# Performance work log

Hardware: AMD Instinct MI355X
Metric: run time of the kernel (lower is better)

## Reference

```python
import jax, jax.numpy as jnp
import numpy as np

NTOKEN = 32000
NINP = 400
NHID = 1150
SEQ = 70
BATCH = 16
ODE_STEPS = 2  # fixed-step RK4 stand-in for adaptive odeint on t in [0,1]


def setup_inputs() -> dict:
    key = jax.random.key(0)
    ks = jax.random.split(key, 16)
    f32 = jnp.float32

    def rn(k, shape, s=0.05):
        return (jax.random.normal(k, shape) * s).astype(f32)

    inp = {"tokens": jax.random.randint(ks[0], (SEQ, BATCH), 0, NTOKEN)}
    dims = [(NINP, NHID), (NHID, NHID), (NHID, NINP)]  # (in, hidden) per layer
    for l, (din, dh) in enumerate(dims):
        inp[f"h0_{l}"] = jnp.zeros((BATCH, dh), f32)
        inp[f"c0_{l}"] = jnp.zeros((BATCH, dh), f32)
        inp[f"Wih{l}"] = rn(ks[1 + 2 * l], (4 * dh, din))
        inp[f"Whh{l}"] = rn(ks[2 + 2 * l], (4 * dh, dh))
        inp[f"bih{l}"] = jnp.zeros((4 * dh,), f32)
        inp[f"bhh{l}"] = jnp.zeros((4 * dh,), f32)
    inp["emb"] = jax.random.uniform(ks[8], (NTOKEN, NINP), minval=-0.1, maxval=0.1, dtype=f32)
    inp["decW"] = jax.random.uniform(ks[9], (NTOKEN, NINP), minval=-0.1, maxval=0.1, dtype=f32)
    inp["decb"] = jnp.zeros((NTOKEN,), f32)
    # ODEfunc: ConcatLinear over [t, x] (width NTOKEN+1) -> NINP bottleneck -> NTOKEN
    inp["odeW1"] = rn(ks[10], (NINP, NTOKEN + 1), 0.01)
    inp["odeb1"] = jnp.zeros((NINP,), f32)
    inp["odeW2"] = rn(ks[11], (NTOKEN, NINP), 0.01)
    inp["odeb2"] = jnp.zeros((NTOKEN,), f32)
    return inp


def _lstm_layer(x, h0, c0, Wih, Whh, bih, bhh):
    # x: [S, B, din] -> outputs [S, B, H]; PyTorch gate order i, f, g, o.
    xp = jnp.einsum('sbd,gd->sbg', x, Wih) + bih + bhh  # [S, B, 4H]

    def cell(carry, xpt):
        h, c = carry
        g = xpt + h @ Whh.T
        i, f, gg, o = jnp.split(g, 4, axis=-1)
        c = jax.nn.sigmoid(f) * c + jax.nn.sigmoid(i) * jnp.tanh(gg)
        h = jax.nn.sigmoid(o) * jnp.tanh(c)
        return (h, c), h

    (hT, cT), ys = jax.lax.scan(cell, (h0, c0), xp)
    return ys, hT, cT


def _ode_rk4(x, W1, b1, W2, b2, n_steps):
    # ConcatLinear: column 0 of W1 multiplies t, remaining columns multiply x.
    wt = W1[:, 0]   # [bneck]
    Wx = W1[:, 1:]  # [bneck, NTOKEN]

    def f(t, y):
        h = jax.nn.softplus(y @ Wx.T + t * wt + b1)
        return h @ W2.T + b2

    dt = 1.0 / n_steps
    ts = jnp.arange(n_steps, dtype=x.dtype) * dt

    def step(y, t):
        k1 = f(t, y)
        k2 = f(t + 0.5 * dt, y + 0.5 * dt * k1)
        k3 = f(t + 0.5 * dt, y + 0.5 * dt * k2)
        k4 = f(t + dt, y + dt * k3)
        return y + (dt / 6.0) * (k1 + 2.0 * k2 + 2.0 * k3 + k4), None

    y, _ = jax.lax.scan(step, x, ts)
    return y


def _forward(tokens, h0s, c0s, lstm_params, emb, decW, decb, odeW1, odeb1, odeW2, odeb2):
    x = emb[tokens]  # [S, B, NINP]  (eval mode: all dropouts inactive)
    for l, (Wih, Whh, bih, bhh) in enumerate(lstm_params):
        x, _, _ = _lstm_layer(x, h0s[l], c0s[l], Wih, Whh, bih, bhh)
    logit = x @ decW.T + decb              # [S, B, NTOKEN]; nhidlast==ninp so no latent layer
    flat = logit.reshape(-1, NTOKEN)       # ODEfunc operates on 2D [S*B, NTOKEN]
    trans = _ode_rk4(flat, odeW1, odeb1, odeW2, odeb2, ODE_STEPS)
    prob = jax.nn.softmax(trans, axis=-1)
    log_prob = jnp.log(prob + 1e-8)        # matches torch.log(prob + 1e-8)
    return log_prob.reshape(SEQ, BATCH, NTOKEN)


def reference(tokens, h0_0, c0_0, h0_1, c0_1, h0_2, c0_2,
              Wih0, Whh0, bih0, bhh0, Wih1, Whh1, bih1, bhh1,
              Wih2, Whh2, bih2, bhh2,
              emb, decW, decb, odeW1, odeb1, odeW2, odeb2):
    return _forward(tokens,
                    [h0_0, h0_1, h0_2], [c0_0, c0_1, c0_2],
                    [(Wih0, Whh0, bih0, bhh0),
                     (Wih1, Whh1, bih1, bhh1),
                     (Wih2, Whh2, bih2, bhh2)],
                    emb, decW, decb, odeW1, odeb1, odeW2, odeb2)
```

## Files before the change

kernel.cpp:

```cpp
#include <hip/hip_runtime.h>
#include <math.h>

constexpr int S_   = 70;
constexpr int B_   = 16;
constexpr int SB_  = 1120;
constexpr int NT_  = 32000;
constexpr int W1S_ = 32001;
constexpr int AST  = 424;

typedef __attribute__((ext_vector_type(8))) short bf16x8;
typedef __attribute__((ext_vector_type(4))) float f32x4;

__device__ __forceinline__ float sigm(float x){ return 1.f/(1.f+__expf(-x)); }
__device__ __forceinline__ float softplusf(float x){ return x > 15.f ? x : log1pf(__expf(x)); }

__device__ __forceinline__ unsigned short f2bf(float f){
    union{float f; unsigned u;} c; c.f = f;
    unsigned u = c.u;
    unsigned r = (u + 0x7fffu + ((u >> 16) & 1u)) >> 16;
    return (unsigned short)r;
}
__device__ __forceinline__ float bfu(unsigned short us){
    union{unsigned u; float f;} c; c.u = ((unsigned)us) << 16; return c.f;
}

__global__ __launch_bounds__(256) void cvt_pack_all_k(
    const float* __restrict__ s0, unsigned short* __restrict__ d0,
    const float* __restrict__ s1, unsigned short* __restrict__ d1,
    const float* __restrict__ s2, unsigned short* __restrict__ d2,
    const float* __restrict__ s3, unsigned short* __restrict__ d3,
    const float* __restrict__ s4, unsigned short* __restrict__ d4,
    const float* __restrict__ s5, unsigned short* __restrict__ d5)
{
    int seg = blockIdx.y;
    const float* src; unsigned short* dst; int R, K, Kp;
    switch(seg){
      case 0: src=s0; dst=d0; R=4600; K=400;  Kp=416;  break;
      case 1: src=s1; dst=d1; R=4600; K=1150; Kp=1152; break;
      case 2: src=s2; dst=d2; R=4600; K=1150; Kp=1152; break;
      case 3: src=s3; dst=d3; R=4600; K=1150; Kp=1152; break;
      case 4: src=s4; dst=d4; R=1600; K=1150; Kp=1152; break;
      default:src=s5; dst=d5; R=1600; K=400;  Kp=416;  break;
    }
    long long idx = (long long)blockIdx.x*256 + threadIdx.x;
    long long tot = (long long)R*Kp;
    if (idx >= tot) return;
    int r = (int)(idx / Kp), kk = (int)(idx - (long long)r*Kp);
    float v = (kk < K) ? src[(size_t)r*K + kk] : 0.f;
    dst[idx] = f2bf(v);
}

__global__ __launch_bounds__(256) void cvt_catB2_k(const float* __restrict__ decW,
                                                   const float* __restrict__ odeW2,
                                                   unsigned short* __restrict__ Bbf,
                                                   unsigned short* __restrict__ BbfT)
{
    __shared__ unsigned short tile[32][72];
    int v0 = blockIdx.x*64, n0 = blockIdx.y*32;
    int tx = threadIdx.x & 31;
    int vy = threadIdx.x >> 5;
    #pragma unroll
    for (int i = 0; i < 8; ++i){
        int v = v0 + i*8 + vy;
        int n = n0 + tx;
        float val = (n < 400) ? decW[(size_t)v*400 + n] : odeW2[(size_t)v*400 + (n-400)];
        unsigned short us = f2bf(val);
        tile[tx][v - v0] = us;
        Bbf[(size_t)v*800 + n] = us;
    }
    __syncthreads();
    int vx = threadIdx.x & 63;
    int ny = threadIdx.x >> 6;
    #pragma unroll
    for (int i = 0; i < 8; ++i){
        int n = n0 + i*4 + ny;
        BbfT[(size_t)n*NT_ + v0 + vx] = tile[n - n0][vx];
    }
}

__global__ __launch_bounds__(256) void cvt_wx_k(const float* __restrict__ odeW1,
                                                unsigned short* __restrict__ Wxbf)
{
    long long idx = (long long)blockIdx.x*256 + threadIdx.x;
    if (idx >= (long long)400*NT_) return;
    int m = (int)(idx / NT_), v = (int)(idx - (long long)m*NT_);
    Wxbf[idx] = f2bf(odeW1[(size_t)m*W1S_ + 1 + v]);
}

__global__ __launch_bounds__(256) void embed_bf_k(const int* __restrict__ tok,
                                                  const float* __restrict__ emb,
                                                  unsigned short* __restrict__ x0A)
{
    int t = blockIdx.x;
    __shared__ int tk[16];
    if (threadIdx.x < 16) tk[threadIdx.x] = tok[t*16 + threadIdx.x];
    __syncthreads();
    for (int idx = threadIdx.x; idx < 16*416; idx += 256){
        int b = idx / 416, k = idx - b*416;
        float v = (k < 400) ? emb[(size_t)tk[b]*400 + k] : 0.f;
        x0A[(size_t)t*16*416 + idx] = f2bf(v);
    }
}

__global__ __launch_bounds__(256) void transpose16_k(const float* __restrict__ src,
                                                     float* __restrict__ dst, int dh)
{
    int idx = blockIdx.x*256 + threadIdx.x;
    if (idx < dh*16){ int j = idx >> 4, b = idx & 15; dst[idx] = src[b*dh + j]; }
}

__global__ __launch_bounds__(256) void cvt_h0_k(const float* __restrict__ h0,
                                                unsigned short* __restrict__ hb, int Dh, int SA)
{
    int idx = blockIdx.x*256 + threadIdx.x;
    if (idx >= 16*Dh) return;
    int b = idx / Dh, j = idx - b*Dh;
    hb[(size_t)b*SA + j] = f2bf(h0[idx]);
}

__device__ __forceinline__ void dotseg(const unsigned short* __restrict__ a,
                                       const unsigned short* __restrict__ b,
                                       int s, int e, int kq,
                                       f32x4& c0, f32x4& c1, f32x4& c2, f32x4& c3)
{
    int k0 = s;
    for (; k0 + 128 <= e; k0 += 128){
        bf16x8 a0 = *(const bf16x8*)(a + k0 + kq);
        bf16x8 b0 = *(const bf16x8*)(b + k0 + kq);
        bf16x8 a1 = *(const bf16x8*)(a + k0 + 32 + kq);
        bf16x8 b1 = *(const bf16x8*)(b + k0 + 32 + kq);
        bf16x8 a2 = *(const bf16x8*)(a + k0 + 64 + kq);
        bf16x8 b2 = *(const bf16x8*)(b + k0 + 64 + kq);
        bf16x8 a3 = *(const bf16x8*)(a + k0 + 96 + kq);
        bf16x8 b3 = *(const bf16x8*)(b + k0 + 96 + kq);
        c0 = __builtin_amdgcn_mfma_f32_16x16x32_bf16(a0, b0, c0, 0,0,0);
        c1 = __builtin_amdgcn_mfma_f32_16x16x32_bf16(a1, b1, c1, 0,0,0);
        c2 = __builtin_amdgcn_mfma_f32_16x16x32_bf16(a2, b2, c2, 0,0,0);
        c3 = __builtin_amdgcn_mfma_f32_16x16x32_bf16(a3, b3, c3, 0,0,0);
    }
    int rem = e - k0;
    if (rem >= 32){
        bf16x8 a0 = *(const bf16x8*)(a + k0 + kq);
        bf16x8 b0 = *(const bf16x8*)(b + k0 + kq);
        c0 = __builtin_amdgcn_mfma_f32_16x16x32_bf16(a0, b0, c0, 0,0,0);
    }
    if (rem >= 64){
        bf16x8 a1 = *(const bf16x8*)(a + k0 + 32 + kq);
        bf16x8 b1 = *(const bf16x8*)(b + k0 + 32 + kq);
        c1 = __builtin_amdgcn_mfma_f32_16x16x32_bf16(a1, b1, c1, 0,0,0);
    }
    if (rem >= 96){
        bf16x8 a2 = *(const bf16x8*)(a + k0 + 64 + kq);
        bf16x8 b2 = *(const bf16x8*)(b + k0 + 64 + kq);
        c2 = __builtin_amdgcn_mfma_f32_16x16x32_bf16(a2, b2, c2, 0,0,0);
    }
}

__global__ __launch_bounds__(1024) void xproj0_k(const unsigned short* __restrict__ x0A,
                                                 const unsigned short* __restrict__ Wih0p,
                                                 unsigned short* __restrict__ xp0)
{
    int jt = blockIdx.x, t = blockIdx.y;
    int j0 = jt*16;
    int lane = threadIdx.x & 63, w = threadIdx.x >> 6;
    int gate = w & 3, seg = w >> 2;
    int am = lane & 15, kq = (lane >> 4)*8, jn = lane & 15;
    int jrow = j0 + jn; if (jrow > 1149) jrow = 1149;

    const unsigned short* ax = x0A + (size_t)t*16*416 + (size_t)am*416;
    const unsigned short* wx = Wih0p + (size_t)(gate*1150 + jrow)*416;
    int nk = 416 >> 5;
    int q0 = ((nk*seg) >> 2) << 5, q1 = ((nk*(seg+1)) >> 2) << 5;
    f32x4 c0v={0.f,0.f,0.f,0.f},c1v={0.f,0.f,0.f,0.f},c2v={0.f,0.f,0.f,0.f},c3v={0.f,0.f,0.f,0.f};
    dotseg(ax, wx, q0, q1, kq, c0v, c1v, c2v, c3v);
    f32x4 acc = (c0v + c1v) + (c2v + c3v);

    __shared__ float g16[16][16][17];
    int bm = (lane >> 4)*4;
    #pragma unroll
    for (int r = 0; r < 4; ++r) g16[w][bm + r][jn] = acc[r];
    __syncthreads();
    if (threadIdx.x < 256){
        int jl = threadIdx.x >> 4, b = threadIdx.x & 15;
        int j = j0 + jl;
        if (j < 1150){
            unsigned short* xp = xp0 + (size_t)t*4600*16;
            #pragma unroll
            for (int g = 0; g < 4; ++g){
                float s = g16[g][b][jl] + g16[g+4][b][jl] + g16[g+8][b][jl] + g16[g+12][b][jl];
                xp[((size_t)(g*1150 + j))*16 + b] = f2bf(s);
            }
        }
    }
}

__global__ __launch_bounds__(1024) void lstm_step2_k(int u,
    unsigned short* __restrict__ ys0A, unsigned short* __restrict__ ys1A,
    float* __restrict__ x3,
    unsigned short* __restrict__ h0b, float* __restrict__ c0,
    unsigned short* __restrict__ h1b, float* __restrict__ c1,
    unsigned short* __restrict__ h2b, float* __restrict__ c2,
    const unsigned short* __restrict__ Whh0p, const float* __restrict__ bih0, const float* __restrict__ bhh0,
    const unsigned short* __restrict__ Wih1p, const unsigned short* __restrict__ Whh1p,
    const float* __restrict__ bih1, const float* __restrict__ bhh1,
    const unsigned short* __restrict__ Wih2p, const unsigned short* __restrict__ Whh2p,
    const float* __restrict__ bih2, const float* __restrict__ bhh2,
    const unsigned short* __restrict__ xp0,
    unsigned short* __restrict__ xp1, unsigned short* __restrict__ xp2)
{
    int blk = blockIdx.x;
    int role, jt;
    if      (blk < 72) { role = 0; jt = blk; }
    else if (blk < 144){ role = 1; jt = blk - 72; }
    else if (blk < 216){ role = 2; jt = blk - 144; }
    else if (blk < 241){ role = 3; jt = blk - 216; }
    else               { role = 4; jt = blk - 241; }
    int t = u - role;
    if (t < 0 || t >= S_) return;
    int j0 = jt*16;

    int lane = threadIdx.x & 63, w = threadIdx.x >> 6;
    int gate = w & 3, seg = w >> 2;
    int am = lane & 15, kq = (lane >> 4)*8, jn = lane & 15;

    __shared__ float g16[16][16][17];

    if (role == 1 || role == 3){
        const unsigned short *A, *Wi; int Dh; unsigned short* xp;
        if (role == 1){ A = ys0A + (size_t)t*16*1152; Wi = Wih1p; Dh = 1150; xp = xp1 + (size_t)t*4600*16; }
        else          { A = ys1A + (size_t)t*16*1152; Wi = Wih2p; Dh = 400;  xp = xp2 + (size_t)t*1600*16; }
        int jrow = j0 + jn; if (jrow > Dh-1) jrow = Dh-1;
        const unsigned short* ax = A + (size_t)am*1152;
        const unsigned short* wx = Wi + (size_t)(gate*Dh + jrow)*1152;
        int nk = 1152 >> 5;
        int q0 = ((nk*seg) >> 2) << 5, q1 = ((nk*(seg+1)) >> 2) << 5;
        f32x4 c0v={0.f,0.f,0.f,0.f},c1v={0.f,0.f,0.f,0.f},c2v={0.f,0.f,0.f,0.f},c3v={0.f,0.f,0.f,0.f};
        dotseg(ax, wx, q0, q1, kq, c0v, c1v, c2v, c3v);
        f32x4 acc = (c0v + c1v) + (c2v + c3v);
        int bm = (lane >> 4)*4;
        #pragma unroll
        for (int r = 0; r < 4; ++r) g16[w][bm + r][jn] = acc[r];
        __syncthreads();
        if (threadIdx.x < 256){
            int jl = threadIdx.x >> 4, b = threadIdx.x & 15;
            int j = j0 + jl;
            if (j < Dh){
                #pragma unroll
                for (int g = 0; g < 4; ++g){
                    float s = g16[g][b][jl] + g16[g+4][b][jl] + g16[g+8][b][jl] + g16[g+12][b][jl];
                    xp[((size_t)(g*Dh + j))*16 + b] = f2bf(s);
                }
            }
        }
    } else {
        const unsigned short *Ah, *Wh, *xp;
        const float *bih, *bhh;
        float *cst, *x3o = nullptr;
        unsigned short *yo = nullptr, *hrec;
        int Dh, SAh, Kh;
        if (role == 0){
            Ah = h0b + (size_t)(t&1)*16*1152; SAh = 1152; Kh = 1152;
            Wh = Whh0p; bih = bih0; bhh = bhh0; Dh = 1150;
            cst = c0; hrec = h0b + (size_t)((t+1)&1)*16*1152;
            yo = ys0A + (size_t)t*16*1152;
            xp = xp0 + (size_t)t*4600*16;
        } else if (role == 2){
            Ah = h1b + (size_t)(t&1)*16*1152; SAh = 1152; Kh = 1152;
            Wh = Whh1p; bih = bih1; bhh = bhh1; Dh = 1150;
            cst = c1; hrec = h1b + (size_t)((t+1)&1)*16*1152;
            yo = ys1A + (size_t)t*16*1152;
            xp = xp1 + (size_t)t*4600*16;
        } else {
            Ah = h2b + (size_t)(t&1)*16*416; SAh = 416; Kh = 416;
            Wh = Whh2p; bih = bih2; bhh = bhh2; Dh = 400;
            cst = c2; hrec = h2b + (size_t)((t+1)&1)*16*416;
            x3o = x3 + (size_t)t*16*400;
            xp = xp2 + (size_t)t*1600*16;
        }
        int jrow = j0 + jn; if (jrow > Dh-1) jrow = Dh-1;
        const unsigned short* ah = Ah + (size_t)am*SAh;
        const unsigned short* wh = Wh + (size_t)(gate*Dh + jrow)*SAh;
        int nk = Kh >> 5;
        int q0 = ((nk*seg) >> 2) << 5, q1 = ((nk*(seg+1)) >> 2) << 5;
        f32x4 c0v={0.f,0.f,0.f,0.f},c1v={0.f,0.f,0.f,0.f},c2v={0.f,0.f,0.f,0.f},c3v={0.f,0.f,0.f,0.f};
        dotseg(ah, wh, q0, q1, kq, c0v, c1v, c2v, c3v);
        f32x4 acc = (c0v + c1v) + (c2v + c3v);
        int bm = (lane >> 4)*4;
        #pragma unroll
        for (int r = 0; r < 4; ++r) g16[w][bm + r][jn] = acc[r];
        __syncthreads();
        if (threadIdx.x < 256){
            int jl = threadIdx.x >> 4, b = threadIdx.x & 15;
            int j = j0 + jl;
            if (j < Dh){
                float pi = g16[0][b][jl] + g16[4][b][jl] + g16[8][b][jl]  + g16[12][b][jl]
                         + bfu(xp[((size_t)(0*Dh + j))*16 + b]) + bih[j]      + bhh[j];
                float pf = g16[1][b][jl] + g16[5][b][jl] + g16[9][b][jl]  + g16[13][b][jl]
                         + bfu(xp[((size_t)(1*Dh + j))*16 + b]) + bih[Dh+j]   + bhh[Dh+j];
                float pg = g16[2][b][jl] + g16[6][b][jl] + g16[10][b][jl] + g16[14][b][jl]
                         + bfu(xp[((size_t)(2*Dh + j))*16 + b]) + bih[2*Dh+j] + bhh[2*Dh+j];
                float po = g16[3][b][jl] + g16[7][b][jl] + g16[11][b][jl] + g16[15][b][jl]
                         + bfu(xp[((size_t)(3*Dh + j))*16 + b]) + bih[3*Dh+j] + bhh[3*Dh+j];
                float cold = cst[j*16 + b];
                float cnew = sigm(pf)*cold + sigm(pi)*tanhf(pg);
                float h    = sigm(po)*tanhf(cnew);
                cst[j*16 + b] = cnew;
                unsigned short hb16 = f2bf(h);
                hrec[(size_t)b*SAh + j] = hb16;
                if (yo)  yo[(size_t)b*1152 + j] = hb16;
                if (x3o) x3o[(size_t)b*400 + j] = h;
            }
        }
    }
}

__global__ __launch_bounds__(256) void vecs_k(const unsigned short* __restrict__ Wxbf,
                                              const float* __restrict__ odeW1,
                                              const float* __restrict__ decb,
                                              const float* __restrict__ b2v,
                                              float* __restrict__ dvec,
                                              float* __restrict__ bvec,
                                              float* __restrict__ wtd)
{
    int jrow = blockIdx.x;
    __shared__ float r1[256], r2[256];
    const unsigned short* wx = Wxbf + (size_t)jrow*NT_;
    float s1 = 0.f, s2 = 0.f;
    for (int v = threadIdx.x; v < NT_; v += 256){
        float w = bfu(wx[v]); s1 += w*decb[v]; s2 += w*b2v[v];
    }
    r1[threadIdx.x] = s1; r2[threadIdx.x] = s2; __syncthreads();
    for (int s = 128; s > 0; s >>= 1){
        if (threadIdx.x < s){ r1[threadIdx.x] += r1[threadIdx.x+s]; r2[threadIdx.x] += r2[threadIdx.x+s]; }
        __syncthreads();
    }
    if (threadIdx.x == 0){ dvec[jrow] = r1[0]; bvec[jrow] = r2[0]; wtd[jrow] = odeW1[(size_t)jrow*W1S_]; }
}

__global__ __launch_bounds__(256) void gemm_odeT_k(
    const unsigned short* __restrict__ Wxbf,
    const unsigned short* __restrict__ BbfT,
    float* __restrict__ partials)
{
    __shared__ unsigned short As[128*44];
    __shared__ unsigned short Bs[128*44];
    int n0 = blockIdx.x*128, m0 = blockIdx.y*128, v0 = blockIdx.z*2000;
    int tid = threadIdx.x;
    int lane = tid & 63, wid = tid >> 6;
    int wr = wid >> 1, wc = wid & 1;
    f32x4 acc[4][4] = {};

    int srow = tid >> 1;
    int sk   = (tid & 1) * 16;
    int mL = m0 + srow; if (mL > 399) mL = 399;
    int nL = n0 + srow; if (nL > 799) nL = 799;
    const unsigned short* ap = Wxbf + (size_t)mL*NT_ + v0 + sk;
    const unsigned short* bp = BbfT + (size_t)nL*NT_ + v0 + sk;

    for (int k0 = 0; k0 < 2000; k0 += 32){
        uint4 av0 = *(const uint4*)(ap + k0);
        uint4 av1 = *(const uint4*)(ap + k0 + 8);
        uint4 bv0 = *(const uint4*)(bp + k0);
        uint4 bv1 = *(const uint4*)(bp + k0 + 8);

        __syncthreads();
        *(uint4*)&As[srow*44 + sk]     = av0;
        *(uint4*)&As[srow*44 + sk + 8] = av1;
        *(uint4*)&Bs[srow*44 + sk]     = bv0;
        *(uint4*)&Bs[srow*44 + sk + 8] = bv1;
        __syncthreads();

        int kq = (lane >> 4) * 8;
        int rA = wr*64 + (lane & 15);
        int rB = wc*64 + (lane & 15);
        bf16x8 af[4], bfv[4];
        #pragma unroll
        for (int f = 0; f < 4; ++f){
            af[f]  = *(const bf16x8*)&As[(rA + f*16)*44 + kq];
            bfv[f] = *(const bf16x8*)&Bs[(rB + f*16)*44 + kq];
        }
        #pragma unroll
        for (int fm = 0; fm < 4; ++fm)
            #pragma unroll
            for (int fn = 0; fn < 4; ++fn)
                acc[fm][fn] = __builtin_amdgcn_mfma_f32_16x16x32_bf16(af[fm], bfv[fn], acc[fm][fn], 0, 0, 0);
    }

    float* op = partials + (size_t)blockIdx.z*320000;
    int cm = (lane >> 4) * 4;
    int cn = lane & 15;
    #pragma unroll
    for (int fm = 0; fm < 4; ++fm){
        int mrow0 = m0 + wr*64 + fm*16 + cm;
        #pragma unroll
        for (int fn = 0; fn < 4; ++fn){
            int n = n0 + wc*64 + fn*16 + cn;
            if (n >= 800) continue;
            #pragma unroll
            for (int r = 0; r < 4; ++r){
                int mr = mrow0 + r;
                if (mr < 400) op[mr*800 + n] = acc[fm][fn][r];
            }
        }
    }
}

__global__ __launch_bounds__(256) void reduce16bf_k(const float* __restrict__ p,
                                                    unsigned short* __restrict__ Qbf,
                                                    unsigned short* __restrict__ Pbf)
{
    int i = blockIdx.x*256 + threadIdx.x;
    if (i >= 320000) return;
    float s = 0.f;
    #pragma unroll
    for (int k = 0; k < 16; ++k) s += p[(size_t)k*320000 + i];
    int m = i / 800, n = i - m*800;
    if (n < 400) Qbf[m*416 + n] = f2bf(s);
    else         Pbf[m*416 + (n-400)] = f2bf(s);
}

__global__ __launch_bounds__(512) void ode_rk4_k(
    const float* __restrict__ x3,
    const unsigned short* __restrict__ Qbf,
    const unsigned short* __restrict__ Pbf,
    const float* __restrict__ dvec, const float* __restrict__ bvec,
    const float* __restrict__ wtd, const float* __restrict__ b1,
    unsigned short* __restrict__ Abf)
{
    __shared__ unsigned short Al[16*AST];
    int m0 = blockIdx.x*16;
    int tid = threadIdx.x;
    int lane = tid & 63, ng = tid >> 6;
    int cm = (lane >> 4)*4;
    int cn = lane & 15;
    int kq = (lane >> 4)*8;

    #pragma unroll
    for (int i = 0; i < 13; ++i){
        int idx = i*512 + tid;
        if (idx < 6400){
            int m = idx / 400, k = idx - m*400;
            unsigned short us = f2bf(x3[(size_t)(m0+m)*400 + k]);
            Al[m*AST + k] = us;
            Abf[(size_t)(m0+m)*800 + k] = us;
        }
    }
    if (tid < 256){ Al[(tid>>4)*AST + 400 + (tid & 15)] = 0; }
    __syncthreads();

    float gy[4][4], hacc[4][4], comb[4][4];
    float vd[4], vb[4], vw[4], v1[4];
    #pragma unroll
    for (int i = 0; i < 4; ++i){
        int nt = ng + 8*i;
        if (nt < 25){
            int n = nt*16 + cn;
            vd[i] = dvec[n]; vb[i] = bvec[n]; vw[i] = wtd[n]; v1[i] = b1[n];
        } else { vd[i]=0.f; vb[i]=0.f; vw[i]=0.f; v1[i]=0.f; }
        #pragma unroll
        for (int r = 0; r < 4; ++r) hacc[i][r] = 0.f;
    }

    const unsigned short* arow = &Al[(size_t)cn*AST + kq];
    f32x4 t4[4];
    auto gemmB = [&](const unsigned short* Bb){
        #pragma unroll
        for (int i = 0; i < 4; ++i){
            f32x4 a = {0.f,0.f,0.f,0.f};
            int nt = ng + 8*i;
            if (nt < 25){
                const unsigned short* brow = Bb + (size_t)(nt*16 + cn)*416 + kq;
                #pragma unroll
                for (int k0 = 0; k0 < 416; k0 += 32){
                    bf16x8 av = *(const bf16x8*)(arow + k0);
                    bf16x8 bv = *(const bf16x8*)(brow + k0);
                    a = __builtin_amdgcn_mfma_f32_16x16x32_bf16(av, bv, a, 0,0,0);
                }
            }
            t4[i] = a;
        }
    };
    auto writeA = [&](float vals[4][4]){
        __syncthreads();
        #pragma unroll
        for (int i = 0; i < 4; ++i){
            int nt = ng + 8*i;
            if (nt < 25){
                int n = nt*16 + cn;
                #pragma unroll
                for (int r = 0; r < 4; ++r)
                    Al[(cm + r)*AST + n] = f2bf(vals[i][r]);
            }
        }
        __syncthreads();
    };

    gemmB(Qbf);
    #pragma unroll
    for (int i = 0; i < 4; ++i)
        #pragma unroll
        for (int r = 0; r < 4; ++r) gy[i][r] = t4[i][r] + vd[i];

    const float dt = 0.5f;
    for (int st = 0; st < 2; ++st){
        float t0 = st * dt;
        float hs[4][4];
        #pragma unroll
        for (int i = 0; i < 4; ++i)
            #pragma unroll
            for (int r = 0; r < 4; ++r){
                float v = softplusf(gy[i][r] + t0*vw[i] + v1[i]);
                hs[i][r] = v; comb[i][r] = v;
            }
        writeA(hs);
        gemmB(Pbf);
        #pragma unroll
        for (int i = 0; i < 4; ++i)
            #pragma unroll
            for (int r = 0; r < 4; ++r){
                float v = softplusf(0.25f*t4[i][r] + gy[i][r] + 0.25f*vb[i] + (t0+0.25f)*vw[i] + v1[i]);
                hs[i][r] = v; comb[i][r] += 2.f*v;
            }
        writeA(hs);
        gemmB(Pbf);
        #pragma unroll
        for (int i = 0; i < 4; ++i)
            #pragma unroll
            for (int r = 0; r < 4; ++r){
                float v = softplusf(0.25f*t4[i][r] + gy[i][r] + 0.25f*vb[i] + (t0+0.25f)*vw[i] + v1[i]);
                hs[i][r] = v; comb[i][r] += 2.f*v;
            }
        writeA(hs);
        gemmB(Pbf);
        #pragma unroll
        for (int i = 0; i < 4; ++i)
            #pragma unroll
            for (int r = 0; r < 4; ++r){
                float v = softplusf(0.5f*t4[i][r] + gy[i][r] + 0.5f*vb[i] + (t0+0.5f)*vw[i] + v1[i]);
                comb[i][r] += v;
            }
        #pragma unroll
        for (int i = 0; i < 4; ++i)
            #pragma unroll
            for (int r = 0; r < 4; ++r){
                float v = comb[i][r] * (1.f/12.f);
                comb[i][r] = v;
                hacc[i][r] += v;
            }
        if (st == 0){
            writeA(comb);
            gemmB(Pbf);
            #pragma unroll
            for (int i = 0; i < 4; ++i)
                #pragma unroll
                for (int r = 0; r < 4; ++r) gy[i][r] += t4[i][r] + dt*vb[i];
        }
    }

    #pragma unroll
    for (int i = 0; i < 4; ++i){
        int nt = ng + 8*i;
        if (nt < 25){
            int n = nt*16 + cn;
            #pragma unroll
            for (int r = 0; r < 4; ++r){
                int m = m0 + cm + r;
                Abf[(size_t)m*800 + 400 + n] = f2bf(hacc[i][r]);
            }
        }
    }
}

__global__ __launch_bounds__(512) void decode_mfma_k(
    const unsigned short* __restrict__ Abf,
    const unsigned short* __restrict__ Bbf,
    const float* __restrict__ decb, const float* __restrict__ b2v,
    float* __restrict__ z)
{
    __shared__ unsigned short As[256*44];
    __shared__ unsigned short Bs[128*44];
    int n0 = blockIdx.x*128, m0 = blockIdx.y*256;
    int tid = threadIdx.x;
    int lane = tid & 63, wid = tid >> 6;
    int wr = wid >> 1, wc = wid & 1;
    f32x4 acc[4][4] = {};

    int srA = tid >> 1, skA = (tid & 1)*16;
    int srB = tid >> 2, skB = (tid & 3)*8;

    for (int k0 = 0; k0 < 800; k0 += 32){
        uint4 av0 = {0,0,0,0}, av1 = {0,0,0,0};
        int m = m0 + srA;
        if (m < SB_){
            const uint4* ap = (const uint4*)(Abf + (size_t)m*800 + k0 + skA);
            av0 = ap[0]; av1 = ap[1];
        }
        uint4 bv = *(const uint4*)(Bbf + (size_t)(n0 + srB)*800 + k0 + skB);

        __syncthreads();
        *(uint4*)&As[srA*44 + skA]     = av0;
        *(uint4*)&As[srA*44 + skA + 8] = av1;
        *(uint4*)&Bs[srB*44 + skB]     = bv;
        __syncthreads();

        int kq = (lane >> 4) * 8;
        int rA = wr*64 + (lane & 15);
        int rB = wc*64 + (lane & 15);
        bf16x8 af[4], bfv[4];
        #pragma unroll
        for (int f = 0; f < 4; ++f){
            af[f]  = *(const bf16x8*)&As[(rA + f*16)*44 + kq];
            bfv[f] = *(const bf16x8*)&Bs[(rB + f*16)*44 + kq];
        }
        #pragma unroll
        for (int fm = 0; fm < 4; ++fm)
            #pragma unroll
            for (int fn = 0; fn < 4; ++fn)
                acc[fm][fn] = __builtin_amdgcn_mfma_f32_16x16x32_bf16(af[fm], bfv[fn], acc[fm][fn], 0, 0, 0);
    }

    int cm = (lane >> 4) * 4;
    int cn = lane & 15;
    #pragma unroll
    for (int fm = 0; fm < 4; ++fm){
        int mrow0 = m0 + wr*64 + fm*16 + cm;
        #pragma unroll
        for (int fn = 0; fn < 4; ++fn){
            int n = n0 + wc*64 + fn*16 + cn;
            float db = decb[n] + b2v[n];
            #pragma unroll
            for (int r = 0; r < 4; ++r){
                int mr = mrow0 + r;
                if (mr < SB_) z[(size_t)mr*NT_ + n] = acc[fm][fn][r] + db;
            }
        }
    }
}

__global__ __launch_bounds__(1024) void softmax_k(float* __restrict__ z)
{
    int r = blockIdx.x;
    float* zr = z + (size_t)r*NT_;
    int tid = threadIdx.x;
    __shared__ float sm[1024];
    float4 v[8];
    float mx = -1e30f;
    #pragma unroll
    for (int i = 0; i < 8; ++i){
        int base = i*4096 + tid*4;
        if (base < NT_){
            v[i] = *(const float4*)(zr + base);
            mx = fmaxf(mx, fmaxf(fmaxf(v[i].x, v[i].y), fmaxf(v[i].z, v[i].w)));
        } else {
            v[i].x = v[i].y = v[i].z = v[i].w = 0.f;
        }
    }
    sm[tid] = mx; __syncthreads();
    for (int s = 512; s > 0; s >>= 1){
        if (tid < s) sm[tid] = fmaxf(sm[tid], sm[tid+s]);
        __syncthreads();
    }
    mx = sm[0]; __syncthreads();
    float sum = 0.f;
    #pragma unroll
    for (int i = 0; i < 8; ++i){
        int base = i*4096 + tid*4;
        if (base < NT_){
            sum += __expf(v[i].x - mx) + __expf(v[i].y - mx)
                 + __expf(v[i].z - mx) + __expf(v[i].w - mx);
        }
    }
    sm[tid] = sum; __syncthreads();
    for (int s = 512; s > 0; s >>= 1){
        if (tid < s) sm[tid] += sm[tid+s];
        __syncthreads();
    }
    float sinv = 1.f / sm[0];
    #pragma unroll
    for (int i = 0; i < 8; ++i){
        int base = i*4096 + tid*4;
        if (base < NT_){
            float4 o;
            o.x = logf(__expf(v[i].x - mx)*sinv + 1e-8f);
            o.y = logf(__expf(v[i].y - mx)*sinv + 1e-8f);
            o.z = logf(__expf(v[i].z - mx)*sinv + 1e-8f);
            o.w = logf(__expf(v[i].w - mx)*sinv + 1e-8f);
            *(float4*)(zr + base) = o;
        }
    }
}

extern "C" void kernel_launch(void* const* d_in, const int* in_sizes, int n_in,
                              void* d_out, int out_size, void* d_ws, size_t ws_size,
                              hipStream_t stream)
{
    const int*   tokens = (const int*)  d_in[0];
    const float* h0_0 = (const float*)d_in[1];
    const float* c0_0 = (const float*)d_in[2];
    const float* Wih0 = (const float*)d_in[3];
    const float* Whh0 = (const float*)d_in[4];
    const float* bih0 = (const float*)d_in[5];
    const float* bhh0 = (const float*)d_in[6];
    const float* h0_1 = (const float*)d_in[7];
    const float* c0_1 = (const float*)d_in[8];
    const float* Wih1 = (const float*)d_in[9];
    const float* Whh1 = (const float*)d_in[10];
    const float* bih1 = (const float*)d_in[11];
    const float* bhh1 = (const float*)d_in[12];
    const float* h0_2 = (const float*)d_in[13];
    const float* c0_2 = (const float*)d_in[14];
    const float* Wih2 = (const float*)d_in[15];
    const float* Whh2 = (const float*)d_in[16];
    const float* bih2 = (const float*)d_in[17];
    const float* bhh2 = (const float*)d_in[18];
    const float* emb  = (const float*)d_in[19];
    const float* decW = (const float*)d_in[20];
    const float* decb = (const float*)d_in[21];
    const float* odeW1= (const float*)d_in[22];
    const float* odeb1= (const float*)d_in[23];
    const float* odeW2= (const float*)d_in[24];
    const float* odeb2= (const float*)d_in[25];

    float* w = (float*)d_ws;
    size_t off = 0;
    auto alloc = [&](size_t n){ float* p = w + off; off += n; return p; };
    auto allocU = [&](size_t nUsh){ return (unsigned short*)alloc(nUsh/2); };
    unsigned short* x0A  = allocU((size_t)S_*16*416);
    unsigned short* ys0A = allocU((size_t)S_*16*1152);
    unsigned short* ys1A = allocU((size_t)S_*16*1152);
    float* x3   = alloc((size_t)SB_*400);
    unsigned short* h0b = allocU((size_t)2*16*1152); float* c0b = alloc(1152*16);
    unsigned short* h1b = allocU((size_t)2*16*1152); float* c1b = alloc(1152*16);
    unsigned short* h2b = allocU((size_t)2*16*416);  float* c2b = alloc(416*16);
    unsigned short* Qbf = allocU((size_t)416*416);
    unsigned short* Pbf = allocU((size_t)416*416);
    float* dvec = alloc(512);
    float* bvec = alloc(512);
    float* wtd  = alloc(512);
    unsigned short* xp0 = allocU((size_t)S_*4600*16);
    unsigned short* xp1 = allocU((size_t)S_*4600*16);
    unsigned short* xp2 = allocU((size_t)S_*1600*16);
    float* partials = alloc((size_t)16*320000);
    unsigned short* Wih0p = allocU((size_t)4600*416);
    unsigned short* Whh0p = allocU((size_t)4600*1152);
    unsigned short* Wih1p = allocU((size_t)4600*1152);
    unsigned short* Whh1p = allocU((size_t)4600*1152);
    unsigned short* Wih2p = allocU((size_t)1600*1152);
    unsigned short* Whh2p = allocU((size_t)1600*416);
    unsigned short* Abf   = allocU((size_t)SB_*800);
    unsigned short* Bbf   = allocU((size_t)NT_*800);
    unsigned short* BbfT  = allocU((size_t)800*NT_);
    unsigned short* Wxbf  = allocU((size_t)400*NT_);
    (void)ws_size; (void)in_sizes; (void)n_in; (void)out_size;

    float* zout = (float*)d_out;

    hipMemsetAsync(ys0A, 0, (size_t)S_*16*1152*2, stream);
    hipMemsetAsync(ys1A, 0, (size_t)S_*16*1152*2, stream);
    hipMemsetAsync(h0b,  0, (size_t)2*16*1152*2, stream);
    hipMemsetAsync(h1b,  0, (size_t)2*16*1152*2, stream);
    hipMemsetAsync(h2b,  0, (size_t)2*16*416*2, stream);
    hipMemsetAsync(Qbf,  0, (size_t)416*416*2, stream);
    hipMemsetAsync(Pbf,  0, (size_t)416*416*2, stream);

    auto cvtgrid = [](long long n){ return (unsigned)((n + 255) / 256); };
    cvt_pack_all_k<<<dim3(cvtgrid((long long)4600*1152), 6), 256, 0, stream>>>(
        Wih0, Wih0p, Whh0, Whh0p, Wih1, Wih1p, Whh1, Whh1p, Wih2, Wih2p, Whh2, Whh2p);
    cvt_catB2_k<<<dim3(500, 25), 256, 0, stream>>>(decW, odeW2, Bbf, BbfT);
    cvt_wx_k<<<cvtgrid((long long)400*NT_), 256, 0, stream>>>(odeW1, Wxbf);

    embed_bf_k<<<S_, 256, 0, stream>>>(tokens, emb, x0A);
    cvt_h0_k<<<(16*1150+255)/256, 256, 0, stream>>>(h0_0, h0b, 1150, 1152);
    cvt_h0_k<<<(16*1150+255)/256, 256, 0, stream>>>(h0_1, h1b, 1150, 1152);
    cvt_h0_k<<<(16*400+255)/256,  256, 0, stream>>>(h0_2, h2b, 400, 416);
    transpose16_k<<<(1150*16+255)/256, 256, 0, stream>>>(c0_0, c0b, 1150);
    transpose16_k<<<(1150*16+255)/256, 256, 0, stream>>>(c0_1, c1b, 1150);
    transpose16_k<<<(400*16+255)/256,  256, 0, stream>>>(c0_2, c2b, 400);

    xproj0_k<<<dim3(72, 70), 1024, 0, stream>>>(x0A, Wih0p, xp0);

    for (int u = 0; u < S_ + 4; ++u)
        lstm_step2_k<<<266, 1024, 0, stream>>>(u, ys0A, ys1A, x3,
            h0b, c0b, h1b, c1b, h2b, c2b,
            Whh0p, bih0, bhh0, Wih1p, Whh1p, bih1, bhh1, Wih2p, Whh2p, bih2, bhh2,
            xp0, xp1, xp2);

    vecs_k<<<400, 256, 0, stream>>>(Wxbf, odeW1, decb, odeb2, dvec, bvec, wtd);
    gemm_odeT_k<<<dim3(7,4,16), 256, 0, stream>>>(Wxbf, BbfT, partials);
    reduce16bf_k<<<(320000+255)/256, 256, 0, stream>>>(partials, Qbf, Pbf);

    ode_rk4_k<<<70, 512, 0, stream>>>(x3, Qbf, Pbf, dvec, bvec, wtd, odeb1, Abf);

    decode_mfma_k<<<dim3(250,5), 512, 0, stream>>>(Abf, Bbf, decb, odeb2, zout);
    softmax_k<<<SB_, 1024, 0, stream>>>(zout);
}
```

Before: 1.583 ms.

## Fold bias vectors into ODE GEMM, swizzle block order, store logits as bf16

Appends decb and odeb2 as two extra columns of the transposed B operand, so the ODE precompute GEMM also produces dvec and bvec. This removes the separate vecs_k pass over Wx, and the reduce kernel now also writes those vectors and wtd. The ODE GEMM and decode GEMM launch orders are remapped so neighbouring blocks land on the same XCD for L2 reuse. Decode logits are written as a bf16 scratch buffer (reusing BbfT) and softmax reads bf16, halving intermediate traffic at the cost of logit precision before softmax.

```diff
diff --git a/kernel.cpp b/kernel.cpp
--- a/kernel.cpp
+++ b/kernel.cpp
@@ -7,6 +7,8 @@
 constexpr int NT_  = 32000;
 constexpr int W1S_ = 32001;
 constexpr int AST  = 424;
+constexpr int NO_  = 802;
+constexpr int NOS  = 816;
 
 typedef __attribute__((ext_vector_type(8))) short bf16x8;
 typedef __attribute__((ext_vector_type(4))) float f32x4;
@@ -52,6 +54,8 @@
 
 __global__ __launch_bounds__(256) void cvt_catB2_k(const float* __restrict__ decW,
                                                    const float* __restrict__ odeW2,
+                                                   const float* __restrict__ decb,
+                                                   const float* __restrict__ b2v,
                                                    unsigned short* __restrict__ Bbf,
                                                    unsigned short* __restrict__ BbfT)
 {
@@ -63,10 +67,15 @@
     for (int i = 0; i < 8; ++i){
         int v = v0 + i*8 + vy;
         int n = n0 + tx;
-        float val = (n < 400) ? decW[(size_t)v*400 + n] : odeW2[(size_t)v*400 + (n-400)];
+        float val;
+        if      (n < 400) val = decW[(size_t)v*400 + n];
+        else if (n < 800) val = odeW2[(size_t)v*400 + (n-400)];
+        else if (n == 800) val = decb[v];
+        else if (n == 801) val = b2v[v];
+        else               val = 0.f;
         unsigned short us = f2bf(val);
         tile[tx][v - v0] = us;
-        Bbf[(size_t)v*800 + n] = us;
+        if (n < 800) Bbf[(size_t)v*800 + n] = us;
     }
     __syncthreads();
     int vx = threadIdx.x & 63;
@@ -74,7 +83,7 @@
     #pragma unroll
     for (int i = 0; i < 8; ++i){
         int n = n0 + i*4 + ny;
-        BbfT[(size_t)n*NT_ + v0 + vx] = tile[n - n0][vx];
+        if (n < NO_) BbfT[(size_t)n*NT_ + v0 + vx] = tile[n - n0][vx];
     }
 }
 
@@ -314,29 +323,6 @@
     }
 }
 
-__global__ __launch_bounds__(256) void vecs_k(const unsigned short* __restrict__ Wxbf,
-                                              const float* __restrict__ odeW1,
-                                              const float* __restrict__ decb,
-                                              const float* __restrict__ b2v,
-                                              float* __restrict__ dvec,
-                                              float* __restrict__ bvec,
-                                              float* __restrict__ wtd)
-{
-    int jrow = blockIdx.x;
-    __shared__ float r1[256], r2[256];
-    const unsigned short* wx = Wxbf + (size_t)jrow*NT_;
-    float s1 = 0.f, s2 = 0.f;
-    for (int v = threadIdx.x; v < NT_; v += 256){
-        float w = bfu(wx[v]); s1 += w*decb[v]; s2 += w*b2v[v];
-    }
-    r1[threadIdx.x] = s1; r2[threadIdx.x] = s2; __syncthreads();
-    for (int s = 128; s > 0; s >>= 1){
-        if (threadIdx.x < s){ r1[threadIdx.x] += r1[threadIdx.x+s]; r2[threadIdx.x] += r2[threadIdx.x+s]; }
-        __syncthreads();
-    }
-    if (threadIdx.x == 0){ dvec[jrow] = r1[0]; bvec[jrow] = r2[0]; wtd[jrow] = odeW1[(size_t)jrow*W1S_]; }
-}
-
 __global__ __launch_bounds__(256) void gemm_odeT_k(
     const unsigned short* __restrict__ Wxbf,
     const unsigned short* __restrict__ BbfT,
@@ -344,7 +330,11 @@
 {
     __shared__ unsigned short As[128*44];
     __shared__ unsigned short Bs[128*44];
-    int n0 = blockIdx.x*128, m0 = blockIdx.y*128, v0 = blockIdx.z*2000;
+    int lin = blockIdx.x + 7*(blockIdx.y + 4*blockIdx.z);
+    int swz = (lin & 7)*56 + (lin >> 3);
+    int xt = swz % 7, rem = swz / 7;
+    int yt = rem & 3, zt = rem >> 2;
+    int n0 = xt*128, m0 = yt*128, v0 = zt*2000;
     int tid = threadIdx.x;
     int lane = tid & 63, wid = tid >> 6;
     int wr = wid >> 1, wc = wid & 1;
@@ -353,7 +343,7 @@
     int srow = tid >> 1;
     int sk   = (tid & 1) * 16;
     int mL = m0 + srow; if (mL > 399) mL = 399;
-    int nL = n0 + srow; if (nL > 799) nL = 799;
+    int nL = n0 + srow; if (nL > NO_-1) nL = NO_-1;
     const unsigned short* ap = Wxbf + (size_t)mL*NT_ + v0 + sk;
     const unsigned short* bp = BbfT + (size_t)nL*NT_ + v0 + sk;
 
@@ -386,7 +376,7 @@
                 acc[fm][fn] = __builtin_amdgcn_mfma_f32_16x16x32_bf16(af[fm], bfv[fn], acc[fm][fn], 0, 0, 0);
     }
 
-    float* op = partials + (size_t)blockIdx.z*320000;
+    float* op = partials + (size_t)zt*400*NOS;
     int cm = (lane >> 4) * 4;
     int cn = lane & 15;
     #pragma unroll
@@ -395,28 +385,35 @@
         #pragma unroll
         for (int fn = 0; fn < 4; ++fn){
             int n = n0 + wc*64 + fn*16 + cn;
-            if (n >= 800) continue;
+            if (n >= NO_) continue;
             #pragma unroll
             for (int r = 0; r < 4; ++r){
                 int mr = mrow0 + r;
-                if (mr < 400) op[mr*800 + n] = acc[fm][fn][r];
-            }
-        }
-    }
-}
-
-__global__ __launch_bounds__(256) void reduce16bf_k(const float* __restrict__ p,
-                                                    unsigned short* __restrict__ Qbf,
-                                                    unsigned short* __restrict__ Pbf)
+                if (mr < 400) op[mr*NOS + n] = acc[fm][fn][r];
+            }
+        }
+    }
+}
+
+__global__ __launch_bounds__(256) void reduce16v_k(const float* __restrict__ p,
+                                                   const float* __restrict__ odeW1,
+                                                   unsigned short* __restrict__ Qbf,
+                                                   unsigned short* __restrict__ Pbf,
+                                                   float* __restrict__ dvec,
+                                                   float* __restrict__ bvec,
+                                                   float* __restrict__ wtd)
 {
     int i = blockIdx.x*256 + threadIdx.x;
-    if (i >= 320000) return;
+    if (i < 400) wtd[i] = odeW1[(size_t)i*W1S_];
+    if (i >= 400*NO_) return;
+    int m = i / NO_, n = i - m*NO_;
     float s = 0.f;
     #pragma unroll
-    for (int k = 0; k < 16; ++k) s += p[(size_t)k*320000 + i];
-    int m = i / 800, n = i - m*800;
-    if (n < 400) Qbf[m*416 + n] = f2bf(s);
-    else         Pbf[m*416 + (n-400)] = f2bf(s);
+    for (int k = 0; k < 16; ++k) s += p[(size_t)k*400*NOS + m*NOS + n];
+    if      (n < 400) Qbf[m*416 + n] = f2bf(s);
+    else if (n < 800) Pbf[m*416 + (n-400)] = f2bf(s);
+    else if (n == 800) dvec[m] = s;
+    else               bvec[m] = s;
 }
 
 __global__ __launch_bounds__(512) void ode_rk4_k(
@@ -575,11 +572,15 @@
     const unsigned short* __restrict__ Abf,
     const unsigned short* __restrict__ Bbf,
     const float* __restrict__ decb, const float* __restrict__ b2v,
-    float* __restrict__ z)
+    unsigned short* __restrict__ zb)
 {
     __shared__ unsigned short As[256*44];
     __shared__ unsigned short Bs[128*44];
-    int n0 = blockIdx.x*128, m0 = blockIdx.y*256;
+    int lin = blockIdx.y + 5*blockIdx.x;
+    int xcd = lin & 7, idx = lin >> 3;
+    int swz = (xcd < 2 ? xcd*157 : 2*157 + (xcd-2)*156) + idx;
+    int mt = swz % 5, ntile = swz / 5;
+    int n0 = ntile*128, m0 = mt*256;
     int tid = threadIdx.x;
     int lane = tid & 63, wid = tid >> 6;
     int wr = wid >> 1, wc = wid & 1;
@@ -631,16 +632,18 @@
             #pragma unroll
             for (int r = 0; r < 4; ++r){
                 int mr = mrow0 + r;
-                if (mr < SB_) z[(size_t)mr*NT_ + n] = acc[fm][fn][r] + db;
-            }
-        }
-    }
-}
-
-__global__ __launch_bounds__(1024) void softmax_k(float* __restrict__ z)
+                if (mr < SB_) zb[(size_t)mr*NT_ + n] = f2bf(acc[fm][fn][r] + db);
+            }
+        }
+    }
+}
+
+__global__ __launch_bounds__(1024) void softmax_k(const unsigned short* __restrict__ zb,
+                                                  float* __restrict__ zout)
 {
     int r = blockIdx.x;
-    float* zr = z + (size_t)r*NT_;
+    const unsigned short* zr = zb + (size_t)r*NT_;
+    float* zo = zout + (size_t)r*NT_;
     int tid = threadIdx.x;
     __shared__ float sm[1024];
     float4 v[8];
@@ -649,7 +652,8 @@
     for (int i = 0; i < 8; ++i){
         int base = i*4096 + tid*4;
         if (base < NT_){
-            v[i] = *(const float4*)(zr + base);
+            ushort4 u = *(const ushort4*)(zr + base);
+            v[i].x = bfu(u.x); v[i].y = bfu(u.y); v[i].z = bfu(u.z); v[i].w = bfu(u.w);
             mx = fmaxf(mx, fmaxf(fmaxf(v[i].x, v[i].y), fmaxf(v[i].z, v[i].w)));
         } else {
             v[i].x = v[i].y = v[i].z = v[i].w = 0.f;
@@ -685,7 +689,7 @@
             o.y = logf(__expf(v[i].y - mx)*sinv + 1e-8f);
             o.z = logf(__expf(v[i].z - mx)*sinv + 1e-8f);
             o.w = logf(__expf(v[i].w - mx)*sinv + 1e-8f);
-            *(float4*)(zr + base) = o;
+            *(float4*)(zo + base) = o;
         }
     }
 }
@@ -740,7 +744,7 @@
     unsigned short* xp0 = allocU((size_t)S_*4600*16);
     unsigned short* xp1 = allocU((size_t)S_*4600*16);
     unsigned short* xp2 = allocU((size_t)S_*1600*16);
-    float* partials = alloc((size_t)16*320000);
+    float* partials = alloc((size_t)16*400*NOS);
     unsigned short* Wih0p = allocU((size_t)4600*416);
     unsigned short* Whh0p = allocU((size_t)4600*1152);
     unsigned short* Wih1p = allocU((size_t)4600*1152);
@@ -749,9 +753,11 @@
     unsigned short* Whh2p = allocU((size_t)1600*416);
     unsigned short* Abf   = allocU((size_t)SB_*800);
     unsigned short* Bbf   = allocU((size_t)NT_*800);
-    unsigned short* BbfT  = allocU((size_t)800*NT_);
+    unsigned short* BbfT  = allocU((size_t)808*NT_);
     unsigned short* Wxbf  = allocU((size_t)400*NT_);
     (void)ws_size; (void)in_sizes; (void)n_in; (void)out_size;
+
+    unsigned short* zb = BbfT;
 
     float* zout = (float*)d_out;
 
@@ -766,7 +772,7 @@
     auto cvtgrid = [](long long n){ return (unsigned)((n + 255) / 256); };
     cvt_pack_all_k<<<dim3(cvtgrid((long long)4600*1152), 6), 256, 0, stream>>>(
         Wih0, Wih0p, Whh0, Whh0p, Wih1, Wih1p, Whh1, Whh1p, Wih2, Wih2p, Whh2, Whh2p);
-    cvt_catB2_k<<<dim3(500, 25), 256, 0, stream>>>(decW, odeW2, Bbf, BbfT);
+    cvt_catB2_k<<<dim3(500, 26), 256, 0, stream>>>(decW, odeW2, decb, odeb2, Bbf, BbfT);
     cvt_wx_k<<<cvtgrid((long long)400*NT_), 256, 0, stream>>>(odeW1, Wxbf);
 
     embed_bf_k<<<S_, 256, 0, stream>>>(tokens, emb, x0A);
@@ -785,12 +791,11 @@
             Whh0p, bih0, bhh0, Wih1p, Whh1p, bih1, bhh1, Wih2p, Whh2p, bih2, bhh2,
             xp0, xp1, xp2);
 
-    vecs_k<<<400, 256, 0, stream>>>(Wxbf, odeW1, decb, odeb2, dvec, bvec, wtd);
     gemm_odeT_k<<<dim3(7,4,16), 256, 0, stream>>>(Wxbf, BbfT, partials);
-    reduce16bf_k<<<(320000+255)/256, 256, 0, stream>>>(partials, Qbf, Pbf);
+    reduce16v_k<<<(400*NO_+255)/256, 256, 0, stream>>>(partials, odeW1, Qbf, Pbf, dvec, bvec, wtd);
 
     ode_rk4_k<<<70, 512, 0, stream>>>(x3, Qbf, Pbf, dvec, bvec, wtd, odeb1, Abf);
 
-    decode_mfma_k<<<dim3(250,5), 512, 0, stream>>>(Abf, Bbf, decb, odeb2, zout);
-    softmax_k<<<SB_, 1024, 0, stream>>>(zout);
-}
+    decode_mfma_k<<<dim3(250,5), 512, 0, stream>>>(Abf, Bbf, decb, odeb2, zb);
+    softmax_k<<<SB_, 1024, 0, stream>>>(zb, zout);
+}
```

New measurement: 1.505 ms. -4.9%, faster.
